# Optimization experiments

Hardware: AMD Instinct MI355X
Metric: run time of the kernel (lower is better)

Reference implementation:

```python
import jax, jax.numpy as jnp
import numpy as np

D_MODEL = 1024
NUM_HEADS = 16
HEAD_DIM = D_MODEL // NUM_HEADS
SCALE = HEAD_DIM ** -0.5
LN_EPS = 1e-5
Q_EPS = 1e-5


def bit_quant(W):
    # BitNet b1.58 ternary weight quantization with straight-through estimator.
    gamma = jnp.mean(jnp.abs(W))
    Wq = jnp.clip(jnp.round(W / (gamma + Q_EPS)), -1.0, 1.0) * gamma
    return W + jax.lax.stop_gradient(Wq - W)


def layer_norm(x, gamma, beta):
    mu = jnp.mean(x, axis=-1, keepdims=True)
    var = jnp.mean(jnp.square(x - mu), axis=-1, keepdims=True)
    return (x - mu) * jax.lax.rsqrt(var + LN_EPS) * gamma + beta


def setup_inputs() -> dict:
    key = jax.random.key(0)
    ks = jax.random.split(key, 8)
    B, T, T_ctx, C = 4, 1024, 2048, D_MODEL
    w_std = C ** -0.5
    return {
        "x": jax.random.normal(ks[0], (B, T, C), jnp.float32),
        "context": jax.random.normal(ks[1], (B, T_ctx, C), jnp.float32),
        "Wq": jax.random.normal(ks[2], (C, C), jnp.float32) * w_std,
        "bq": jnp.zeros((C,), jnp.float32),
        "Wk": jax.random.normal(ks[3], (C, C), jnp.float32) * w_std,
        "bk": jnp.zeros((C,), jnp.float32),
        "Wv": jax.random.normal(ks[4], (C, C), jnp.float32) * w_std,
        "bv": jnp.zeros((C,), jnp.float32),
        "Wo": jax.random.normal(ks[5], (C, C), jnp.float32) * w_std,
        "bo": jnp.zeros((C,), jnp.float32),
        "ln_gamma": jnp.ones((C,), jnp.float32),
        "ln_beta": jnp.zeros((C,), jnp.float32),
    }


def reference(x, context, Wq, bq, Wk, bk, Wv, bv, Wo, bo, ln_gamma, ln_beta):
    B, T, C = x.shape
    T_ctx = context.shape[1]
    residual = x
    xn = layer_norm(x, ln_gamma, ln_beta)
    # BitNet-quantized projections (torch Linear: y = x @ W.T + b)
    q = xn @ bit_quant(Wq).T + bq                      # [B,T,C]
    k = context @ bit_quant(Wk).T + bk                 # [B,T_ctx,C]
    v = context @ bit_quant(Wv).T + bv                 # [B,T_ctx,C]
    q = q.reshape(B, T, NUM_HEADS, HEAD_DIM)
    k = k.reshape(B, T_ctx, NUM_HEADS, HEAD_DIM)
    v = v.reshape(B, T_ctx, NUM_HEADS, HEAD_DIM)
    scores = jnp.einsum("bqhd,bkhd->bhqk", q, k) * SCALE   # [B,H,T,T_ctx]
    probs = jax.nn.softmax(scores, axis=-1)
    out = jnp.einsum("bhqk,bkhd->bqhd", probs, v).reshape(B, T, C)
    return residual + (out @ bit_quant(Wo).T + bo)
```

## Files before the change

kernel.cpp:

```cpp
#include <hip/hip_runtime.h>
#include <hip/hip_bf16.h>

typedef __attribute__((ext_vector_type(8))) short s8x;
typedef __attribute__((ext_vector_type(4))) float f4x;
typedef unsigned short u16;
typedef unsigned int u32;

#define T_ 1024
#define TC_ 2048
#define SCLOG2E 0.1803368801111243f

#define WAIT_VM(n) asm volatile("s_waitcnt vmcnt(" #n ")" ::: "memory")

__device__ __forceinline__ u16 f2bf(float f) {
    u32 u = __float_as_uint(f);
    return (u16)((u + 0x7fffu + ((u >> 16) & 1u)) >> 16);
}

#if defined(__has_builtin)
#if __has_builtin(__builtin_amdgcn_cvt_pk_bf16_f32)
#define HAVE_PK 1
#endif
#if __has_builtin(__builtin_amdgcn_permlane16_swap) && __has_builtin(__builtin_amdgcn_permlane32_swap)
#define HAVE_PLSWAP 1
#endif
#endif

__device__ __forceinline__ u32 pack2bf(float a, float b) {
#ifdef HAVE_PK
    typedef __attribute__((ext_vector_type(2))) __bf16 bf2t;
    bf2t r = __builtin_amdgcn_cvt_pk_bf16_f32(a, b);
    u32 u;
    __builtin_memcpy(&u, &r, 4);
    return u;
#else
    return (u32)f2bf(a) | ((u32)f2bf(b) << 16);
#endif
}

__device__ __forceinline__ void pswap32(u32& a, u32& b) {
#ifdef HAVE_PLSWAP
    typedef __attribute__((ext_vector_type(2))) unsigned int u2x;
    u2x r = __builtin_amdgcn_permlane32_swap(a, b, false, false);
    a = r.x; b = r.y;
#else
    asm("v_permlane32_swap_b32 %0, %1" : "+v"(a), "+v"(b));
#endif
}
__device__ __forceinline__ void pswap16(u32& a, u32& b) {
#ifdef HAVE_PLSWAP
    typedef __attribute__((ext_vector_type(2))) unsigned int u2x;
    u2x r = __builtin_amdgcn_permlane16_swap(a, b, false, false);
    a = r.x; b = r.y;
#else
    asm("v_permlane16_swap_b32 %0, %1" : "+v"(a), "+v"(b));
#endif
}

__device__ __forceinline__ void gload16(const void* g, void* l) {
    __builtin_amdgcn_global_load_lds((const __attribute__((address_space(1))) u32*)g,
                                     (__attribute__((address_space(3))) u32*)l, 16, 0, 0);
}

__global__ __launch_bounds__(256) void absmean_k(const float* __restrict__ W0, const float* __restrict__ W1,
                                                 const float* __restrict__ W2, const float* __restrict__ W3,
                                                 float* __restrict__ gsum) {
    int wi = blockIdx.y;
    const float* W = (wi == 0) ? W0 : (wi == 1) ? W1 : (wi == 2) ? W2 : W3;
    const int n4 = (1024 * 1024) / 4;
    float s = 0.f;
    int stride = gridDim.x * blockDim.x;
    for (int i = blockIdx.x * blockDim.x + threadIdx.x; i < n4; i += stride) {
        float4 v = ((const float4*)W)[i];
        s += fabsf(v.x) + fabsf(v.y) + fabsf(v.z) + fabsf(v.w);
    }
#pragma unroll
    for (int off = 32; off; off >>= 1) s += __shfl_down(s, off, 64);
    __shared__ float ps[4];
    if ((threadIdx.x & 63) == 0) ps[threadIdx.x >> 6] = s;
    __syncthreads();
    if (threadIdx.x == 0) atomicAdd(gsum + wi, ps[0] + ps[1] + ps[2] + ps[3]);
}

__global__ __launch_bounds__(256) void prep_k(
        const float* __restrict__ x, const float* __restrict__ lng, const float* __restrict__ lnb,
        u16* __restrict__ xn,
        const float* __restrict__ ctx, u16* __restrict__ ctxb,
        const float* __restrict__ W0, const float* __restrict__ W1,
        const float* __restrict__ W2, const float* __restrict__ W3,
        u16* __restrict__ D0, u16* __restrict__ D1, u16* __restrict__ D2, u16* __restrict__ D3,
        const float* __restrict__ gsum) {
    __shared__ float ps[8];
    int bx = blockIdx.x, t = threadIdx.x;
    if (bx < 4096) {
        int row = bx;
        float4 xv = ((const float4*)(x + (long)row * 1024))[t];
        float s = xv.x + xv.y + xv.z + xv.w;
        float s2 = xv.x * xv.x + xv.y * xv.y + xv.z * xv.z + xv.w * xv.w;
#pragma unroll
        for (int off = 32; off; off >>= 1) { s += __shfl_down(s, off, 64); s2 += __shfl_down(s2, off, 64); }
        if ((t & 63) == 0) { ps[t >> 6] = s; ps[4 + (t >> 6)] = s2; }
        __syncthreads();
        float S = ps[0] + ps[1] + ps[2] + ps[3];
        float S2 = ps[4] + ps[5] + ps[6] + ps[7];
        float mu = S * (1.f / 1024.f);
        float var = S2 * (1.f / 1024.f) - mu * mu;
        float rstd = rsqrtf(var + 1e-5f);
        float4 gv = ((const float4*)lng)[t];
        float4 bv = ((const float4*)lnb)[t];
        uint2 o;
        o.x = pack2bf((xv.x - mu) * rstd * gv.x + bv.x, (xv.y - mu) * rstd * gv.y + bv.y);
        o.y = pack2bf((xv.z - mu) * rstd * gv.z + bv.z, (xv.w - mu) * rstd * gv.w + bv.w);
        ((uint2*)(xn + (long)row * 1024))[t] = o;
    } else if (bx < 12288) {
        int i = (bx - 4096) * 256 + t;
        float4 v = ((const float4*)ctx)[i];
        uint2 o = {pack2bf(v.x, v.y), pack2bf(v.z, v.w)};
        ((uint2*)ctxb)[i] = o;
    } else {
        int wi = (bx - 12288) >> 10;
        const float* W = (wi == 0) ? W0 : (wi == 1) ? W1 : (wi == 2) ? W2 : W3;
        u16* D = (wi == 0) ? D0 : (wi == 1) ? D1 : (wi == 2) ? D2 : D3;
        float inv = 1.0f / (gsum[wi] * (1.0f / 1048576.0f) + 1e-5f);
        int i = ((bx - 12288) & 1023) * 256 + t;
        float4 wv = ((const float4*)W)[i];
        uint2 o;
        o.x = pack2bf(fminf(1.f, fmaxf(-1.f, rintf(wv.x * inv))),
                      fminf(1.f, fmaxf(-1.f, rintf(wv.y * inv))));
        o.y = pack2bf(fminf(1.f, fmaxf(-1.f, rintf(wv.z * inv))),
                      fminf(1.f, fmaxf(-1.f, rintf(wv.w * inv))));
        ((uint2*)D)[i] = o;
    }
}

__global__ __launch_bounds__(256) void gemm_fused(
        const u16* __restrict__ xn, const u16* __restrict__ ctxb,
        const u16* __restrict__ wtq, const u16* __restrict__ wtk, const u16* __restrict__ wtv,
        const float* __restrict__ bq, const float* __restrict__ bk, const float* __restrict__ bv,
        const float* __restrict__ gsum,
        u16* __restrict__ qb, u16* __restrict__ kb, u16* __restrict__ vtb) {
    __shared__ __align__(16) char smem[49152];
    int tid = threadIdx.x;
    int w = tid >> 6, l = tid & 63, lq = l & 15, lh = l >> 4;
    int wm = (w >> 1) * 64, wn = (w & 1) * 64;
    int bx = blockIdx.x;
    int xcd = bx & 7;
    int prob, m0, n0, gidx;
    const u16 *A, *Wt;
    const float* bias;
    float sc;
    if (bx < 256) {
        int local = bx >> 3;
        prob = 0; A = xn; Wt = wtq; bias = bq; sc = SCLOG2E; gidx = 0;
        m0 = (xcd * 4 + (local & 3)) * 128;
        n0 = (local >> 2) * 128;
    } else {
        int b = bx - 256;
        int local3 = b >> 3;
        int kv = local3 & 1;
        int idx = local3 >> 1;
        prob = 1 + kv; A = ctxb;
        Wt = kv ? wtv : wtk; bias = kv ? bv : bk; sc = 1.0f; gidx = 1 + kv;
        m0 = (xcd * 8 + (idx & 7)) * 128;
        n0 = (idx >> 3) * 128;
    }
    int sp = tid >> 3, ss = tid & 7;
    int st = ss ^ (sp & 7);
    int r0 = sp * 2 + (st >> 2), c0 = st & 3;
    const u16* Ag0 = A + (long)(m0 + r0) * 1024 + c0 * 8;
    const u16* Ag1 = Ag0 + 64 * 1024;
    const u16* Bg0 = Wt + (long)(n0 + r0) * 1024 + c0 * 8;
    const u16* Bg1 = Bg0 + 64 * 1024;
    int aoff[4], boff[4];
#pragma unroll
    for (int i = 0; i < 4; i++) {
        int ar = wm + i * 16 + lq, ap = ar >> 1;
        aoff[i] = ap * 128 + (((((ar & 1) << 2) | lh) ^ (ap & 7)) * 16);
        int br = wn + i * 16 + lq, bp = br >> 1;
        boff[i] = bp * 128 + (((((br & 1) << 2) | lh) ^ (bp & 7)) * 16);
    }
    f4x acc[4][4] = {};
#define STAGE_G(kt, buf)                                                   \
    {                                                                      \
        char* Ad = smem + (buf) * 16384;                                   \
        char* Bd = Ad + 8192;                                              \
        gload16(Ag0 + (kt) * 32, Ad + tid * 16);                           \
        gload16(Ag1 + (kt) * 32, Ad + 4096 + tid * 16);                    \
        gload16(Bg0 + (kt) * 32, Bd + tid * 16);                           \
        gload16(Bg1 + (kt) * 32, Bd + 4096 + tid * 16);                    \
    }
    STAGE_G(0, 0);
    STAGE_G(1, 1);
#pragma unroll
    for (int kt = 0; kt < 32; kt++) {
        if (kt < 31) { WAIT_VM(4); } else { WAIT_VM(0); }
        __builtin_amdgcn_s_barrier();
        if (kt + 2 < 32) STAGE_G(kt + 2, (kt + 2) % 3);
        const char* Ac = smem + (kt % 3) * 16384;
        const char* Bc = Ac + 8192;
        s8x af[4], bfr[4];
#pragma unroll
        for (int i = 0; i < 4; i++) {
            af[i] = *(const s8x*)(Ac + aoff[i]);
            bfr[i] = *(const s8x*)(Bc + boff[i]);
        }
#pragma unroll
        for (int i = 0; i < 4; i++)
#pragma unroll
            for (int j = 0; j < 4; j++)
                acc[i][j] = __builtin_amdgcn_mfma_f32_16x16x32_bf16(af[i], bfr[j], acc[i][j], 0, 0, 0);
    }
    float gamma = gsum[gidx] * (1.0f / 1048576.0f) * sc;
    if (prob < 2) {
        u16* outq = (prob == 0) ? qb : kb;
        int tshift = (prob == 0) ? 10 : 11;
        int tmask = (1 << tshift) - 1;
#pragma unroll
        for (int i = 0; i < 4; i++) {
            int gr = m0 + wm + i * 16 + lh * 4;
#pragma unroll
            for (int j = 0; j < 4; j++) {
                int gc = n0 + wn + j * 16 + lq;
                float bb = bias[gc] * sc;
                int h = gc >> 6, d = gc & 63;
#pragma unroll
                for (int r = 0; r < 4; r++) {
                    int row = gr + r;
                    int bidx = row >> tshift, tt = row & tmask;
                    outq[((((long)(bidx * 16 + h)) << tshift) + tt) * 64 + d] = f2bf(acc[i][j][r] * gamma + bb);
                }
            }
        }
    } else {
        __syncthreads();
        char* Ct = smem;
#pragma unroll
        for (int i = 0; i < 4; i++) {
            int tt = wm + i * 16 + lh * 4;
#pragma unroll
            for (int j = 0; j < 4; j++) {
                int c = wn + j * 16 + lq;
                float bb = bias[n0 + c];
                uint2 pk;
                pk.x = pack2bf(acc[i][j][0] * gamma + bb, acc[i][j][1] * gamma + bb);
                pk.y = pack2bf(acc[i][j][2] * gamma + bb, acc[i][j][3] * gamma + bb);
                int slot = (tt >> 3) ^ (c & 15);
                *(uint2*)(Ct + c * 256 + slot * 16 + (tt & 7) * 2) = pk;
            }
        }
        __syncthreads();
        int bb2 = m0 >> 11, t0 = m0 & 2047;
#pragma unroll
        for (int it = 0; it < 8; it++) {
            int e = it * 256 + tid;
            int c = e >> 4, ch = e & 15;
            int slot = ch ^ (c & 15);
            s8x v = *(const s8x*)(Ct + c * 256 + slot * 16);
            int gcg = n0 + c;
            int h = gcg >> 6, d = gcg & 63;
            *(s8x*)(vtb + ((long)((bb2 * 16 + h) * 64 + d)) * TC_ + t0 + ch * 8) = v;
        }
    }
}

__global__ __launch_bounds__(256) void gemm_o(const u16* __restrict__ A, const u16* __restrict__ Wt,
                                              const float* __restrict__ bias, const float* __restrict__ gsum,
                                              const float* __restrict__ residual, float* __restrict__ outr) {
    __shared__ __align__(16) char smem[36864];
    int tid = threadIdx.x;
    int w = tid >> 6, l = tid & 63, lq = l & 15, lh = l >> 4;
    int wm = (w >> 1) * 64, wn = (w & 1) * 32;
    int bx = blockIdx.x;
    int xcd = bx & 7, local = bx >> 3;
    int m0 = (xcd * 4 + (local & 3)) * 128;
    int n0 = (local >> 2) * 64;
    int sp = tid >> 3, ss = tid & 7;
    int st = ss ^ (sp & 7);
    int r0 = sp * 2 + (st >> 2), c0 = st & 3;
    const u16* Ag0 = A + (long)(m0 + r0) * 1024 + c0 * 8;
    const u16* Ag1 = Ag0 + 64 * 1024;
    const u16* Bg0 = Wt + (long)(n0 + r0) * 1024 + c0 * 8;
    int aoff[4], boff[2];
#pragma unroll
    for (int i = 0; i < 4; i++) {
        int ar = wm + i * 16 + lq, ap = ar >> 1;
        aoff[i] = ap * 128 + (((((ar & 1) << 2) | lh) ^ (ap & 7)) * 16);
    }
#pragma unroll
    for (int j = 0; j < 2; j++) {
        int br = wn + j * 16 + lq, bp = br >> 1;
        boff[j] = bp * 128 + (((((br & 1) << 2) | lh) ^ (bp & 7)) * 16);
    }
    f4x acc[4][2] = {};
#define STAGE_O(kt, buf)                                                   \
    {                                                                      \
        char* Ad = smem + (buf) * 12288;                                   \
        char* Bd = Ad + 8192;                                              \
        gload16(Ag0 + (kt) * 32, Ad + tid * 16);                           \
        gload16(Ag1 + (kt) * 32, Ad + 4096 + tid * 16);                    \
        gload16(Bg0 + (kt) * 32, Bd + tid * 16);                           \
    }
    STAGE_O(0, 0);
    STAGE_O(1, 1);
#pragma unroll
    for (int kt = 0; kt < 32; kt++) {
        if (kt < 31) { WAIT_VM(3); } else { WAIT_VM(0); }
        __builtin_amdgcn_s_barrier();
        if (kt + 2 < 32) STAGE_O(kt + 2, (kt + 2) % 3);
        const char* Ac = smem + (kt % 3) * 12288;
        const char* Bc = Ac + 8192;
        s8x af[4], bfr[2];
#pragma unroll
        for (int i = 0; i < 4; i++) af[i] = *(const s8x*)(Ac + aoff[i]);
#pragma unroll
        for (int j = 0; j < 2; j++) bfr[j] = *(const s8x*)(Bc + boff[j]);
#pragma unroll
        for (int i = 0; i < 4; i++)
#pragma unroll
            for (int j = 0; j < 2; j++)
                acc[i][j] = __builtin_amdgcn_mfma_f32_16x16x32_bf16(af[i], bfr[j], acc[i][j], 0, 0, 0);
    }
    float gamma = gsum[3] * (1.0f / 1048576.0f);
#pragma unroll
    for (int i = 0; i < 4; i++) {
        int gr = m0 + wm + i * 16 + lh * 4;
#pragma unroll
        for (int j = 0; j < 2; j++) {
            int gc = n0 + wn + j * 16 + lq;
            float bb = bias[gc];
#pragma unroll
            for (int r = 0; r < 4; r++) {
                long idx = (long)(gr + r) * 1024 + gc;
                outr[idx] = residual[idx] + acc[i][j][r] * gamma + bb;
            }
        }
    }
}

__global__ __launch_bounds__(256) void attn_k(const u16* __restrict__ qh, const u16* __restrict__ kh,
                                              const u16* __restrict__ vth, u16* __restrict__ attn) {
    __shared__ __align__(16) char smem[32768];
    int tid = threadIdx.x, w = tid >> 6, l = tid & 63, lq = l & 15, lh = l >> 4;
    int bh = blockIdx.x, q0 = blockIdx.y * 64;
    const u16* qp = qh + ((long)bh * T_ + q0) * 64;
    const u16* kp = kh + (long)bh * TC_ * 64;
    const u16* vp = vth + (long)bh * 64 * TC_;
#pragma unroll
    for (int i = 0; i < 2; i++) {
        int cid = i * 256 + tid;
        int r = cid >> 3, c = (cid & 7) ^ (r & 7);
        gload16(qp + r * 64 + c * 8, smem + cid * 16);
    }
    __syncthreads();
    s8x qf[2];
#pragma unroll
    for (int dh = 0; dh < 2; dh++) {
        int qrow = w * 16 + lq;
        int ch = (dh * 4 + lh) ^ (qrow & 7);
        qf[dh] = *(const s8x*)(smem + qrow * 128 + ch * 16);
    }
    __syncthreads();
#define STAGE_KV(kt, buf)                                                          \
    {                                                                              \
        char* Kb = smem + (buf) * 16384;                                           \
        char* Vb = Kb + 8192;                                                      \
        _Pragma("unroll") for (int i = 0; i < 2; i++) {                            \
            int cid = i * 256 + tid;                                               \
            int r = cid >> 3, c = (cid & 7) ^ (r & 7);                             \
            gload16(kp + ((kt) * 64 + r) * 64 + c * 8, Kb + cid * 16);             \
            gload16(vp + (long)r * TC_ + (kt) * 64 + c * 8, Vb + cid * 16);        \
        }                                                                          \
    }
    STAGE_KV(0, 0);
    f4x oacc[4] = {};
    f4x lrun = {};
    const s8x ones = {16256, 16256, 16256, 16256, 16256, 16256, 16256, 16256};
    for (int kt = 0; kt < TC_ / 64; kt++) {
        __syncthreads();
        if (kt + 1 < TC_ / 64) STAGE_KV(kt + 1, (kt + 1) & 1);
        char* Ksb = smem + (kt & 1) * 16384;
        char* Vsb = Ksb + 8192;
        f4x z[4];
        __builtin_amdgcn_s_setprio(1);
#pragma unroll
        for (int ni = 0; ni < 4; ni++) {
            int kr = ni * 16 + lq;
            s8x a0 = *(const s8x*)(Ksb + kr * 128 + ((lh) ^ (kr & 7)) * 16);
            s8x a1 = *(const s8x*)(Ksb + kr * 128 + ((4 + lh) ^ (kr & 7)) * 16);
            f4x zz = {0.f, 0.f, 0.f, 0.f};
            zz = __builtin_amdgcn_mfma_f32_16x16x32_bf16(a0, qf[0], zz, 0, 0, 0);
            zz = __builtin_amdgcn_mfma_f32_16x16x32_bf16(a1, qf[1], zz, 0, 0, 0);
            z[ni] = zz;
        }
        __builtin_amdgcn_s_setprio(0);
        s8x vf[4][2];
#pragma unroll
        for (int nd = 0; nd < 4; nd++) {
            int vr = nd * 16 + lq;
            vf[nd][0] = *(const s8x*)(Vsb + vr * 128 + ((lh) ^ (vr & 7)) * 16);
            vf[nd][1] = *(const s8x*)(Vsb + vr * 128 + ((4 + lh) ^ (vr & 7)) * 16);
        }
        u32 Wp[4][2];
#pragma unroll
        for (int ni = 0; ni < 4; ni++) {
            Wp[ni][0] = pack2bf(__builtin_amdgcn_exp2f(z[ni][0]), __builtin_amdgcn_exp2f(z[ni][1]));
            Wp[ni][1] = pack2bf(__builtin_amdgcn_exp2f(z[ni][2]), __builtin_amdgcn_exp2f(z[ni][3]));
        }
        u32 a0w = Wp[0][0], a1w = Wp[1][0]; pswap32(a0w, a1w); pswap16(a0w, a1w);
        u32 b0w = Wp[0][1], b1w = Wp[1][1]; pswap32(b0w, b1w); pswap16(b0w, b1w);
        u32 c0w = Wp[2][0], c1w = Wp[3][0]; pswap32(c0w, c1w); pswap16(c0w, c1w);
        u32 d0w = Wp[2][1], d1w = Wp[3][1]; pswap32(d0w, d1w); pswap16(d0w, d1w);
        u32 pw0[4] = {a0w, b0w, a1w, b1w};
        u32 pw1[4] = {c0w, d0w, c1w, d1w};
        s8x pf0, pf1;
        __builtin_memcpy(&pf0, pw0, 16);
        __builtin_memcpy(&pf1, pw1, 16);
        __builtin_amdgcn_s_setprio(1);
        f4x rs = {0.f, 0.f, 0.f, 0.f};
        rs = __builtin_amdgcn_mfma_f32_16x16x32_bf16(pf0, ones, rs, 0, 0, 0);
        rs = __builtin_amdgcn_mfma_f32_16x16x32_bf16(pf1, ones, rs, 0, 0, 0);
#pragma unroll
        for (int r = 0; r < 4; r++) lrun[r] += rs[r];
#pragma unroll
        for (int nd = 0; nd < 4; nd++) {
            oacc[nd] = __builtin_amdgcn_mfma_f32_16x16x32_bf16(pf0, vf[nd][0], oacc[nd], 0, 0, 0);
            oacc[nd] = __builtin_amdgcn_mfma_f32_16x16x32_bf16(pf1, vf[nd][1], oacc[nd], 0, 0, 0);
        }
        __builtin_amdgcn_s_setprio(0);
    }
    int b = bh >> 4, h = bh & 15;
#pragma unroll
    for (int r = 0; r < 4; r++) {
        int q = q0 + w * 16 + lh * 4 + r;
        float rcp = 1.f / lrun[r];
#pragma unroll
        for (int nd = 0; nd < 4; nd++)
            attn[((long)(b * T_ + q)) * 1024 + h * 64 + nd * 16 + lq] = f2bf(oacc[nd][r] * rcp);
    }
}

extern "C" void kernel_launch(void* const* d_in, const int* in_sizes, int n_in,
                              void* d_out, int out_size, void* d_ws, size_t ws_size,
                              hipStream_t stream) {
    const float* x   = (const float*)d_in[0];
    const float* ctx = (const float*)d_in[1];
    const float* Wq  = (const float*)d_in[2];
    const float* bq  = (const float*)d_in[3];
    const float* Wk  = (const float*)d_in[4];
    const float* bk  = (const float*)d_in[5];
    const float* Wv  = (const float*)d_in[6];
    const float* bv  = (const float*)d_in[7];
    const float* Wo  = (const float*)d_in[8];
    const float* bo  = (const float*)d_in[9];
    const float* lng = (const float*)d_in[10];
    const float* lnb = (const float*)d_in[11];
    float* out = (float*)d_out;

    char* ws = (char*)d_ws;
    float* gsum = (float*)ws;
    size_t off = 256;
    u16* wtq  = (u16*)(ws + off); off += (size_t)1024 * 1024 * 2;
    u16* wtk  = (u16*)(ws + off); off += (size_t)1024 * 1024 * 2;
    u16* wtv  = (u16*)(ws + off); off += (size_t)1024 * 1024 * 2;
    u16* wto  = (u16*)(ws + off); off += (size_t)1024 * 1024 * 2;
    u16* ctxb = (u16*)(ws + off); off += (size_t)8192 * 1024 * 2;
    u16* xn   = (u16*)(ws + off); off += (size_t)4096 * 1024 * 2;
    u16* qb_  = (u16*)(ws + off); off += (size_t)4096 * 1024 * 2;
    u16* kb   = (u16*)(ws + off); off += (size_t)8192 * 1024 * 2;
    u16* vtb  = (u16*)(ws + off); off += (size_t)8192 * 1024 * 2;
    u16* attnb = xn;

    hipMemsetAsync(gsum, 0, 16, stream);
    absmean_k<<<dim3(128, 4), 256, 0, stream>>>(Wq, Wk, Wv, Wo, gsum);
    prep_k<<<16384, 256, 0, stream>>>(x, lng, lnb, xn, ctx, ctxb,
                                      Wq, Wk, Wv, Wo, wtq, wtk, wtv, wto, gsum);
    gemm_fused<<<1280, 256, 0, stream>>>(xn, ctxb, wtq, wtk, wtv, bq, bk, bv, gsum, qb_, kb, vtb);
    attn_k<<<dim3(64, 16), 256, 0, stream>>>(qb_, kb, vtb, attnb);
    gemm_o<<<512, 256, 0, stream>>>(attnb, wto, bo, gsum, x, out);
}
```

Measured before the change: 251.8 us.

## Double query rows per attention block to reuse each K/V tile twice

Each attention workgroup now handles 128 query rows instead of 64, with every wave processing two 16-row query sub-blocks against the same staged K/V tile. This halves the global loads of K and V per query and the number of shared-memory staging rounds, which raises arithmetic intensity. In exchange each wave keeps twice as many accumulators and score registers, which may lower occupancy. The grid shrinks to 512 blocks, which may leave compute units less evenly loaded.

```diff
diff --git a/kernel.cpp b/kernel.cpp
--- a/kernel.cpp
+++ b/kernel.cpp
@@ -341,24 +341,26 @@
                                               const u16* __restrict__ vth, u16* __restrict__ attn) {
     __shared__ __align__(16) char smem[32768];
     int tid = threadIdx.x, w = tid >> 6, l = tid & 63, lq = l & 15, lh = l >> 4;
-    int bh = blockIdx.x, q0 = blockIdx.y * 64;
+    int bh = blockIdx.x, q0 = blockIdx.y * 128;
     const u16* qp = qh + ((long)bh * T_ + q0) * 64;
     const u16* kp = kh + (long)bh * TC_ * 64;
     const u16* vp = vth + (long)bh * 64 * TC_;
 #pragma unroll
-    for (int i = 0; i < 2; i++) {
+    for (int i = 0; i < 4; i++) {
         int cid = i * 256 + tid;
         int r = cid >> 3, c = (cid & 7) ^ (r & 7);
         gload16(qp + r * 64 + c * 8, smem + cid * 16);
     }
     __syncthreads();
-    s8x qf[2];
-#pragma unroll
-    for (int dh = 0; dh < 2; dh++) {
-        int qrow = w * 16 + lq;
-        int ch = (dh * 4 + lh) ^ (qrow & 7);
-        qf[dh] = *(const s8x*)(smem + qrow * 128 + ch * 16);
-    }
+    s8x qf[2][2];
+#pragma unroll
+    for (int qb = 0; qb < 2; qb++)
+#pragma unroll
+        for (int dh = 0; dh < 2; dh++) {
+            int qrow = w * 32 + qb * 16 + lq;
+            int ch = (dh * 4 + lh) ^ (qrow & 7);
+            qf[qb][dh] = *(const s8x*)(smem + qrow * 128 + ch * 16);
+        }
     __syncthreads();
 #define STAGE_KV(kt, buf)                                                          \
     {                                                                              \
@@ -372,25 +374,28 @@
         }                                                                          \
     }
     STAGE_KV(0, 0);
-    f4x oacc[4] = {};
-    f4x lrun = {};
+    f4x oacc[2][4] = {};
+    f4x lrun[2] = {};
     const s8x ones = {16256, 16256, 16256, 16256, 16256, 16256, 16256, 16256};
     for (int kt = 0; kt < TC_ / 64; kt++) {
         __syncthreads();
         if (kt + 1 < TC_ / 64) STAGE_KV(kt + 1, (kt + 1) & 1);
         char* Ksb = smem + (kt & 1) * 16384;
         char* Vsb = Ksb + 8192;
-        f4x z[4];
+        f4x z[2][4];
         __builtin_amdgcn_s_setprio(1);
 #pragma unroll
         for (int ni = 0; ni < 4; ni++) {
             int kr = ni * 16 + lq;
             s8x a0 = *(const s8x*)(Ksb + kr * 128 + ((lh) ^ (kr & 7)) * 16);
             s8x a1 = *(const s8x*)(Ksb + kr * 128 + ((4 + lh) ^ (kr & 7)) * 16);
-            f4x zz = {0.f, 0.f, 0.f, 0.f};
-            zz = __builtin_amdgcn_mfma_f32_16x16x32_bf16(a0, qf[0], zz, 0, 0, 0);
-            zz = __builtin_amdgcn_mfma_f32_16x16x32_bf16(a1, qf[1], zz, 0, 0, 0);
-            z[ni] = zz;
+#pragma unroll
+            for (int qb = 0; qb < 2; qb++) {
+                f4x zz = {0.f, 0.f, 0.f, 0.f};
+                zz = __builtin_amdgcn_mfma_f32_16x16x32_bf16(a0, qf[qb][0], zz, 0, 0, 0);
+                zz = __builtin_amdgcn_mfma_f32_16x16x32_bf16(a1, qf[qb][1], zz, 0, 0, 0);
+                z[qb][ni] = zz;
+            }
         }
         __builtin_amdgcn_s_setprio(0);
         s8x vf[4][2];
@@ -400,43 +405,48 @@
             vf[nd][0] = *(const s8x*)(Vsb + vr * 128 + ((lh) ^ (vr & 7)) * 16);
             vf[nd][1] = *(const s8x*)(Vsb + vr * 128 + ((4 + lh) ^ (vr & 7)) * 16);
         }
-        u32 Wp[4][2];
-#pragma unroll
-        for (int ni = 0; ni < 4; ni++) {
-            Wp[ni][0] = pack2bf(__builtin_amdgcn_exp2f(z[ni][0]), __builtin_amdgcn_exp2f(z[ni][1]));
-            Wp[ni][1] = pack2bf(__builtin_amdgcn_exp2f(z[ni][2]), __builtin_amdgcn_exp2f(z[ni][3]));
-        }
-        u32 a0w = Wp[0][0], a1w = Wp[1][0]; pswap32(a0w, a1w); pswap16(a0w, a1w);
-        u32 b0w = Wp[0][1], b1w = Wp[1][1]; pswap32(b0w, b1w); pswap16(b0w, b1w);
-        u32 c0w = Wp[2][0], c1w = Wp[3][0]; pswap32(c0w, c1w); pswap16(c0w, c1w);
-        u32 d0w = Wp[2][1], d1w = Wp[3][1]; pswap32(d0w, d1w); pswap16(d0w, d1w);
-        u32 pw0[4] = {a0w, b0w, a1w, b1w};
-        u32 pw1[4] = {c0w, d0w, c1w, d1w};
-        s8x pf0, pf1;
-        __builtin_memcpy(&pf0, pw0, 16);
-        __builtin_memcpy(&pf1, pw1, 16);
-        __builtin_amdgcn_s_setprio(1);
-        f4x rs = {0.f, 0.f, 0.f, 0.f};
-        rs = __builtin_amdgcn_mfma_f32_16x16x32_bf16(pf0, ones, rs, 0, 0, 0);
-        rs = __builtin_amdgcn_mfma_f32_16x16x32_bf16(pf1, ones, rs, 0, 0, 0);
-#pragma unroll
-        for (int r = 0; r < 4; r++) lrun[r] += rs[r];
-#pragma unroll
-        for (int nd = 0; nd < 4; nd++) {
-            oacc[nd] = __builtin_amdgcn_mfma_f32_16x16x32_bf16(pf0, vf[nd][0], oacc[nd], 0, 0, 0);
-            oacc[nd] = __builtin_amdgcn_mfma_f32_16x16x32_bf16(pf1, vf[nd][1], oacc[nd], 0, 0, 0);
-        }
-        __builtin_amdgcn_s_setprio(0);
+#pragma unroll
+        for (int qb = 0; qb < 2; qb++) {
+            u32 Wp[4][2];
+#pragma unroll
+            for (int ni = 0; ni < 4; ni++) {
+                Wp[ni][0] = pack2bf(__builtin_amdgcn_exp2f(z[qb][ni][0]), __builtin_amdgcn_exp2f(z[qb][ni][1]));
+                Wp[ni][1] = pack2bf(__builtin_amdgcn_exp2f(z[qb][ni][2]), __builtin_amdgcn_exp2f(z[qb][ni][3]));
+            }
+            u32 a0w = Wp[0][0], a1w = Wp[1][0]; pswap32(a0w, a1w); pswap16(a0w, a1w);
+            u32 b0w = Wp[0][1], b1w = Wp[1][1]; pswap32(b0w, b1w); pswap16(b0w, b1w);
+            u32 c0w = Wp[2][0], c1w = Wp[3][0]; pswap32(c0w, c1w); pswap16(c0w, c1w);
+            u32 d0w = Wp[2][1], d1w = Wp[3][1]; pswap32(d0w, d1w); pswap16(d0w, d1w);
+            u32 pw0[4] = {a0w, b0w, a1w, b1w};
+            u32 pw1[4] = {c0w, d0w, c1w, d1w};
+            s8x pf0, pf1;
+            __builtin_memcpy(&pf0, pw0, 16);
+            __builtin_memcpy(&pf1, pw1, 16);
+            __builtin_amdgcn_s_setprio(1);
+            f4x rs = {0.f, 0.f, 0.f, 0.f};
+            rs = __builtin_amdgcn_mfma_f32_16x16x32_bf16(pf0, ones, rs, 0, 0, 0);
+            rs = __builtin_amdgcn_mfma_f32_16x16x32_bf16(pf1, ones, rs, 0, 0, 0);
+#pragma unroll
+            for (int r = 0; r < 4; r++) lrun[qb][r] += rs[r];
+#pragma unroll
+            for (int nd = 0; nd < 4; nd++) {
+                oacc[qb][nd] = __builtin_amdgcn_mfma_f32_16x16x32_bf16(pf0, vf[nd][0], oacc[qb][nd], 0, 0, 0);
+                oacc[qb][nd] = __builtin_amdgcn_mfma_f32_16x16x32_bf16(pf1, vf[nd][1], oacc[qb][nd], 0, 0, 0);
+            }
+            __builtin_amdgcn_s_setprio(0);
+        }
     }
     int b = bh >> 4, h = bh & 15;
 #pragma unroll
-    for (int r = 0; r < 4; r++) {
-        int q = q0 + w * 16 + lh * 4 + r;
-        float rcp = 1.f / lrun[r];
-#pragma unroll
-        for (int nd = 0; nd < 4; nd++)
-            attn[((long)(b * T_ + q)) * 1024 + h * 64 + nd * 16 + lq] = f2bf(oacc[nd][r] * rcp);
-    }
+    for (int qb = 0; qb < 2; qb++)
+#pragma unroll
+        for (int r = 0; r < 4; r++) {
+            int q = q0 + w * 32 + qb * 16 + lh * 4 + r;
+            float rcp = 1.f / lrun[qb][r];
+#pragma unroll
+            for (int nd = 0; nd < 4; nd++)
+                attn[((long)(b * T_ + q)) * 1024 + h * 64 + nd * 16 + lq] = f2bf(oacc[qb][nd][r] * rcp);
+        }
 }
 
 extern "C" void kernel_launch(void* const* d_in, const int* in_sizes, int n_in,
@@ -475,6 +485,6 @@
     prep_k<<<16384, 256, 0, stream>>>(x, lng, lnb, xn, ctx, ctxb,
                                       Wq, Wk, Wv, Wo, wtq, wtk, wtv, wto, gsum);
     gemm_fused<<<1280, 256, 0, stream>>>(xn, ctxb, wtq, wtk, wtv, bq, bk, bv, gsum, qb_, kb, vtb);
-    attn_k<<<dim3(64, 16), 256, 0, stream>>>(qb_, kb, vtb, attnb);
+    attn_k<<<dim3(64, 8), 256, 0, stream>>>(qb_, kb, vtb, attnb);
     gemm_o<<<512, 256, 0, stream>>>(attnb, wto, bo, gsum, x, out);
 }
```

Result: no change. 254.2 us (+1.0%).
